# Performance work log

Measured on AMD Instinct MI355X. Metric: run time of the kernel, lower is better.

## Reference

```python
import jax, jax.numpy as jnp
import numpy as np

DIM = 1024
N_HEADS = 16
SCALE = (DIM // N_HEADS) ** (-0.5)


def setup_inputs() -> dict:
    key = jax.random.key(0)
    kq, kk, kv = jax.random.split(key, 3)
    shape = (4, 16, 2048, 64)  # [B, H, N, Dh]
    q = jax.random.normal(kq, shape, dtype=jnp.float32)
    k = jax.random.normal(kk, shape, dtype=jnp.float32)
    v = jax.random.normal(kv, shape, dtype=jnp.float32)
    return {"q": q, "k": k, "v": v}


def reference(q, k, v):
    # Faithful translation of the torch module, INCLUDING its einsum output
    # subscripts: the second einsum is 'bhnm,bhmd->bhmd' (sums over n, keeps m),
    # exactly as written in the source.
    scores = jnp.einsum('bhnd,bhmd->bhnm', q, k) * SCALE  # [B,H,N,M]
    scores = jax.nn.softmax(scores, axis=-1)
    out = jnp.einsum('bhnm,bhmd->bhmd', scores, v)  # [B,H,M,Dh]
    return out
```

## Files before the change

### kernel.cpp

```cpp
#include <hip/hip_runtime.h>
#include <cstdint>
#include <cstddef>

#define B_    4
#define H_    16
#define N_    2048
#define D_    64
#define BH_   (B_*H_)
#define SCALE 0.125f
#define QSCL  0.18033688011f

#define P_    256
#define T_    128
#define NT    (N_/T_)
#define NP    (N_/P_)
#define TILEB 16384
#define BHB   (NT*TILEB)

typedef __attribute__((ext_vector_type(8))) short bf16x8;
typedef __attribute__((ext_vector_type(4))) float f32x4;

#if __has_builtin(__builtin_amdgcn_exp2f)
#define EXP2(x) __builtin_amdgcn_exp2f(x)
#else
#define EXP2(x) exp2f(x)
#endif

__device__ __forceinline__ short f2bf(float f) {
    union { float f; unsigned u; } x; x.f = f;
    unsigned r = x.u + 0x7FFF + ((x.u >> 16) & 1);
    return (short)(r >> 16);
}

__device__ __forceinline__ size_t swz(int row, int cc) {
    return ((size_t)(row >> 7) * TILEB) + ((row & 127) << 7) + ((cc ^ (row & 7)) << 4);
}

__global__ __launch_bounds__(512)
void mha_convert(const float* __restrict__ q, const float* __restrict__ k,
                 char* __restrict__ qk)
{
    const int gid = blockIdx.x * 512 + threadIdx.x;
    const int half = BH_ * N_ * 8;
    const bool isq = gid < half;
    const float* src = isq ? q : k;
    const float scl = isq ? QSCL : 1.0f;
    char* dst = qk + (isq ? 0 : (size_t)BH_ * BHB);
    const int id = isq ? gid : gid - half;
    const int bh  = id >> 14;
    const int row = (id >> 3) & 2047;
    const int cc  = id & 7;
    const float* p = src + ((size_t)bh * N_ + row) * D_ + cc * 8;
    float4 a = *(const float4*)p;
    float4 b = *(const float4*)(p + 4);
    bf16x8 o;
    o[0] = f2bf(a.x * scl); o[1] = f2bf(a.y * scl);
    o[2] = f2bf(a.z * scl); o[3] = f2bf(a.w * scl);
    o[4] = f2bf(b.x * scl); o[5] = f2bf(b.y * scl);
    o[6] = f2bf(b.z * scl); o[7] = f2bf(b.w * scl);
    *(bf16x8*)(dst + (size_t)bh * BHB + swz(row, cc)) = o;
}

__global__ __launch_bounds__(512)
void mha_rowsum2(const char* __restrict__ qk, float* __restrict__ rinv)
{
    __shared__ __align__(16) char KT[TILEB];

    const int t = threadIdx.x, w = t >> 6, l = t & 63;
    const int wid = (blockIdx.x & 7) * 64 + (blockIdx.x >> 3);
    const int bh = wid / NP, rb = wid % NP;

    const char* Qp = qk + (size_t)bh * BHB;
    const char* Kp = qk + (size_t)BH_ * BHB + (size_t)bh * BHB;

    bf16x8 af[2][2];
    #pragma unroll
    for (int rg = 0; rg < 2; ++rg)
        #pragma unroll
        for (int kh = 0; kh < 2; ++kh) {
            int row = rb * P_ + w * 32 + rg * 16 + (l & 15);
            af[rg][kh] = *(const bf16x8*)(Qp + swz(row, kh * 4 + (l >> 4)));
        }

    float rs[2][4] = {};

    for (int ct = 0; ct < NT; ++ct) {
        __syncthreads();
        const char* src = Kp + (size_t)ct * TILEB;
        *(bf16x8*)(KT + t * 16)        = *(const bf16x8*)(src + t * 16);
        *(bf16x8*)(KT + 8192 + t * 16) = *(const bf16x8*)(src + 8192 + t * 16);
        __syncthreads();

        #pragma unroll
        for (int cj = 0; cj < 8; ++cj) {
            const int krow = cj * 16 + (l & 15);
            const int kb = (krow & 127) << 7;
            bf16x8 b0 = *(const bf16x8*)(KT + kb + (((l >> 4) ^ (krow & 7)) << 4));
            bf16x8 b1 = *(const bf16x8*)(KT + kb + (((4 + (l >> 4)) ^ (krow & 7)) << 4));
            #pragma unroll
            for (int rg = 0; rg < 2; ++rg) {
                f32x4 c = {0.f, 0.f, 0.f, 0.f};
                c = __builtin_amdgcn_mfma_f32_16x16x32_bf16(af[rg][0], b0, c, 0, 0, 0);
                c = __builtin_amdgcn_mfma_f32_16x16x32_bf16(af[rg][1], b1, c, 0, 0, 0);
                rs[rg][0] += EXP2(c[0]);
                rs[rg][1] += EXP2(c[1]);
                rs[rg][2] += EXP2(c[2]);
                rs[rg][3] += EXP2(c[3]);
            }
        }
    }

    #pragma unroll
    for (int rg = 0; rg < 2; ++rg)
        #pragma unroll
        for (int i = 0; i < 4; ++i) {
            rs[rg][i] += __shfl_xor(rs[rg][i], 1);
            rs[rg][i] += __shfl_xor(rs[rg][i], 2);
            rs[rg][i] += __shfl_xor(rs[rg][i], 4);
            rs[rg][i] += __shfl_xor(rs[rg][i], 8);
        }
    if ((l & 15) == 0) {
        #pragma unroll
        for (int rg = 0; rg < 2; ++rg) {
            const int rbase = rb * P_ + w * 32 + rg * 16 + (l >> 4) * 4;
            #pragma unroll
            for (int i = 0; i < 4; ++i)
                rinv[(size_t)bh * N_ + rbase + i] = 1.0f / rs[rg][i];
        }
    }
}

__global__ __launch_bounds__(512)
void mha_colsum2(const char* __restrict__ qk, const float* __restrict__ rinv,
                 const float* __restrict__ v, float* __restrict__ out)
{
    __shared__ __align__(16) char QT[TILEB];
    __shared__ float rv[T_];
    __shared__ float cs[P_];

    const int t = threadIdx.x, w = t >> 6, l = t & 63;
    const int wid = (blockIdx.x & 7) * 64 + (blockIdx.x >> 3);
    const int bh = wid / NP, cb = wid % NP;

    const char* Qp = qk + (size_t)bh * BHB;
    const char* Kp = qk + (size_t)BH_ * BHB + (size_t)bh * BHB;
    const float* Rg = rinv + (size_t)bh * N_;

    bf16x8 kf[2][2];
    #pragma unroll
    for (int rg = 0; rg < 2; ++rg)
        #pragma unroll
        for (int kh = 0; kh < 2; ++kh) {
            int col = cb * P_ + w * 32 + rg * 16 + (l & 15);
            kf[rg][kh] = *(const bf16x8*)(Kp + swz(col, kh * 4 + (l >> 4)));
        }

    float ca[2] = {0.f, 0.f};

    for (int rt = 0; rt < NT; ++rt) {
        __syncthreads();
        const char* src = Qp + (size_t)rt * TILEB;
        *(bf16x8*)(QT + t * 16)        = *(const bf16x8*)(src + t * 16);
        *(bf16x8*)(QT + 8192 + t * 16) = *(const bf16x8*)(src + 8192 + t * 16);
        if (t < T_) rv[t] = Rg[rt * T_ + t];
        __syncthreads();

        #pragma unroll
        for (int rj = 0; rj < 8; ++rj) {
            const int qr = rj * 16 + (l & 15);
            const int qb = (qr & 127) << 7;
            bf16x8 a0 = *(const bf16x8*)(QT + qb + (((l >> 4) ^ (qr & 7)) << 4));
            bf16x8 a1 = *(const bf16x8*)(QT + qb + (((4 + (l >> 4)) ^ (qr & 7)) << 4));
            float4 r4 = *(const float4*)&rv[rj * 16 + (l >> 4) * 4];
            #pragma unroll
            for (int rg = 0; rg < 2; ++rg) {
                f32x4 c = {0.f, 0.f, 0.f, 0.f};
                c = __builtin_amdgcn_mfma_f32_16x16x32_bf16(a0, kf[rg][0], c, 0, 0, 0);
                c = __builtin_amdgcn_mfma_f32_16x16x32_bf16(a1, kf[rg][1], c, 0, 0, 0);
                ca[rg] += EXP2(c[0]) * r4.x + EXP2(c[1]) * r4.y
                        + EXP2(c[2]) * r4.z + EXP2(c[3]) * r4.w;
            }
        }
    }

    #pragma unroll
    for (int rg = 0; rg < 2; ++rg) {
        ca[rg] += __shfl_xor(ca[rg], 16);
        ca[rg] += __shfl_xor(ca[rg], 32);
    }
    if (l < 16) { cs[w * 32 + l] = ca[0]; cs[w * 32 + 16 + l] = ca[1]; }
    __syncthreads();

    const float4* Vg = (const float4*)(v + ((size_t)bh * N_ + cb * P_) * D_);
    float4* Og = (float4*)(out + ((size_t)bh * N_ + cb * P_) * D_);
    #pragma unroll
    for (int i = 0; i < 8; ++i) {
        int id = i * 512 + t;
        float s = cs[id >> 4];
        float4 vv = Vg[id];
        float4 o; o.x = vv.x * s; o.y = vv.y * s; o.z = vv.z * s; o.w = vv.w * s;
        Og[id] = o;
    }
}

#define FTS 128
#define FNT 16

__device__ __forceinline__ bf16x8 cvt8(const float* p) {
    float4 a = *(const float4*)p;
    float4 b = *(const float4*)(p + 4);
    bf16x8 r;
    r[0] = f2bf(a.x); r[1] = f2bf(a.y); r[2] = f2bf(a.z); r[3] = f2bf(a.w);
    r[4] = f2bf(b.x); r[5] = f2bf(b.y); r[6] = f2bf(b.z); r[7] = f2bf(b.w);
    return r;
}
__device__ __forceinline__ void fstage(char* lds, const float* src, int t) {
    #pragma unroll
    for (int i = 0; i < 2; ++i) {
        int ch = i * 512 + t, r = ch >> 3, cc = ch & 7;
        bf16x8 v = cvt8(src + (size_t)r * D_ + cc * 8);
        *(bf16x8*)(lds + r * 128 + ((cc ^ (r & 7)) << 4)) = v;
    }
}
__device__ __forceinline__ bf16x8 fread(const char* lds, int row, int cc) {
    return *(const bf16x8*)(lds + row * 128 + ((cc ^ (row & 7)) << 4));
}

__global__ __launch_bounds__(512)
void mha_rowsum_fb(const float* __restrict__ q, const float* __restrict__ k,
                   float* __restrict__ rinv)
{
    __shared__ __align__(16) char KT[FTS * 128];
    const int t = threadIdx.x, w = t >> 6, l = t & 63;
    const int bh = blockIdx.x / FNT, rb = blockIdx.x % FNT;
    const float* Qg = q + (size_t)bh * N_ * D_;
    const float* Kg = k + (size_t)bh * N_ * D_;
    const int qrow = rb * FTS + w * 16 + (l & 15);
    bf16x8 af[2];
    #pragma unroll
    for (int kh = 0; kh < 2; ++kh)
        af[kh] = cvt8(Qg + (size_t)qrow * D_ + kh * 32 + (l >> 4) * 8);
    float rs[4] = {0.f, 0.f, 0.f, 0.f};
    for (int ct = 0; ct < FNT; ++ct) {
        __syncthreads();
        fstage(KT, Kg + (size_t)ct * FTS * D_, t);
        __syncthreads();
        #pragma unroll
        for (int cj = 0; cj < 8; ++cj) {
            const int krow = cj * 16 + (l & 15);
            f32x4 c = {0.f, 0.f, 0.f, 0.f};
            #pragma unroll
            for (int kh = 0; kh < 2; ++kh)
                c = __builtin_amdgcn_mfma_f32_16x16x32_bf16(af[kh], fread(KT, krow, kh * 4 + (l >> 4)), c, 0, 0, 0);
            rs[0] += __expf(c[0] * SCALE); rs[1] += __expf(c[1] * SCALE);
            rs[2] += __expf(c[2] * SCALE); rs[3] += __expf(c[3] * SCALE);
        }
    }
    #pragma unroll
    for (int i = 0; i < 4; ++i) {
        rs[i] += __shfl_xor(rs[i], 1); rs[i] += __shfl_xor(rs[i], 2);
        rs[i] += __shfl_xor(rs[i], 4); rs[i] += __shfl_xor(rs[i], 8);
    }
    if ((l & 15) == 0) {
        const int rbase = rb * FTS + w * 16 + (l >> 4) * 4;
        #pragma unroll
        for (int i = 0; i < 4; ++i)
            rinv[(size_t)bh * N_ + rbase + i] = 1.0f / rs[i];
    }
}

__global__ __launch_bounds__(512)
void mha_colsum_fb(const float* __restrict__ q, const float* __restrict__ k,
                   const float* __restrict__ v, const float* __restrict__ rinv,
                   float* __restrict__ out)
{
    __shared__ __align__(16) char QT[FTS * 128];
    __shared__ float rv[FTS];
    __shared__ float cs[FTS];
    const int t = threadIdx.x, w = t >> 6, l = t & 63;
    const int bh = blockIdx.x / FNT, cb = blockIdx.x % FNT;
    const float* Qg = q + (size_t)bh * N_ * D_;
    const float* Kg = k + (size_t)bh * N_ * D_;
    const float* Rg = rinv + (size_t)bh * N_;
    const int kcol = cb * FTS + w * 16 + (l & 15);
    bf16x8 kf[2];
    #pragma unroll
    for (int kh = 0; kh < 2; ++kh)
        kf[kh] = cvt8(Kg + (size_t)kcol * D_ + kh * 32 + (l >> 4) * 8);
    float ca = 0.f;
    for (int rt = 0; rt < FNT; ++rt) {
        __syncthreads();
        fstage(QT, Qg + (size_t)rt * FTS * D_, t);
        if (t < FTS) rv[t] = Rg[rt * FTS + t];
        __syncthreads();
        #pragma unroll
        for (int rj = 0; rj < 8; ++rj) {
            const int qr = rj * 16 + (l & 15);
            f32x4 c = {0.f, 0.f, 0.f, 0.f};
            #pragma unroll
            for (int kh = 0; kh < 2; ++kh)
                c = __builtin_amdgcn_mfma_f32_16x16x32_bf16(fread(QT, qr, kh * 4 + (l >> 4)), kf[kh], c, 0, 0, 0);
            float4 r4 = *(const float4*)&rv[rj * 16 + (l >> 4) * 4];
            ca += __expf(c[0] * SCALE) * r4.x + __expf(c[1] * SCALE) * r4.y
                + __expf(c[2] * SCALE) * r4.z + __expf(c[3] * SCALE) * r4.w;
        }
    }
    ca += __shfl_xor(ca, 16); ca += __shfl_xor(ca, 32);
    if (l < 16) cs[w * 16 + l] = ca;
    __syncthreads();
    const float4* Vg = (const float4*)(v + (size_t)bh * N_ * D_ + (size_t)cb * FTS * D_);
    float4* Og = (float4*)(out + (size_t)bh * N_ * D_ + (size_t)cb * FTS * D_);
    #pragma unroll
    for (int i = 0; i < 4; ++i) {
        int id = i * 512 + t;
        float s = cs[id >> 4];
        float4 vv = Vg[id];
        float4 o; o.x = vv.x * s; o.y = vv.y * s; o.z = vv.z * s; o.w = vv.w * s;
        Og[id] = o;
    }
}

extern "C" void kernel_launch(void* const* d_in, const int* in_sizes, int n_in,
                              void* d_out, int out_size, void* d_ws, size_t ws_size,
                              hipStream_t stream)
{
    const float* q = (const float*)d_in[0];
    const float* k = (const float*)d_in[1];
    const float* v = (const float*)d_in[2];
    float* out = (float*)d_out;

    const size_t qkBytes = (size_t)2 * BH_ * BHB;
    const size_t need = qkBytes + (size_t)BH_ * N_ * 4;

    if (ws_size >= need) {
        char* qk = (char*)d_ws;
        float* rinv = (float*)(qk + qkBytes);
        mha_convert<<<dim3(2 * BH_ * N_ * 8 / 512), dim3(512), 0, stream>>>(q, k, qk);
        mha_rowsum2<<<dim3(BH_ * NP), dim3(512), 0, stream>>>(qk, rinv);
        mha_colsum2<<<dim3(BH_ * NP), dim3(512), 0, stream>>>(qk, rinv, v, out);
    } else {
        float* rinv = (float*)d_ws;
        mha_rowsum_fb<<<dim3(BH_ * FNT), dim3(512), 0, stream>>>(q, k, rinv);
        mha_colsum_fb<<<dim3(BH_ * FNT), dim3(512), 0, stream>>>(q, k, v, rinv, out);
    }
}
```

Measured before the change: 108.4 us.

## Double-buffer K/Q tiles via direct global-to-LDS loads and halve rows per block

```diff
diff --git a/kernel.cpp b/kernel.cpp
--- a/kernel.cpp
+++ b/kernel.cpp
@@ -10,10 +10,10 @@
 #define SCALE 0.125f
 #define QSCL  0.18033688011f
 
-#define P_    256
-#define T_    128
-#define NT    (N_/T_)
-#define NP    (N_/P_)
+#define P2    128
+#define T2    128
+#define NT    (N_/T2)
+#define NP2   (N_/P2)
 #define TILEB 16384
 #define BHB   (NT*TILEB)
 
@@ -34,6 +34,12 @@
 
 __device__ __forceinline__ size_t swz(int row, int cc) {
     return ((size_t)(row >> 7) * TILEB) + ((row & 127) << 7) + ((cc ^ (row & 7)) << 4);
+}
+
+__device__ __forceinline__ void gload_lds16(const char* g, char* l) {
+    __builtin_amdgcn_global_load_lds(
+        (const __attribute__((address_space(1))) void*)g,
+        (__attribute__((address_space(3))) void*)l, 16, 0, 0);
 }
 
 __global__ __launch_bounds__(512)
@@ -62,139 +68,137 @@
 }
 
 __global__ __launch_bounds__(512)
-void mha_rowsum2(const char* __restrict__ qk, float* __restrict__ rinv)
-{
-    __shared__ __align__(16) char KT[TILEB];
+void mha_rowsum3(const char* __restrict__ qk, float* __restrict__ rinv)
+{
+    __shared__ __align__(16) char KT[2][TILEB];
 
     const int t = threadIdx.x, w = t >> 6, l = t & 63;
-    const int wid = (blockIdx.x & 7) * 64 + (blockIdx.x >> 3);
-    const int bh = wid / NP, rb = wid % NP;
+    const int wid = (blockIdx.x & 7) * 128 + (blockIdx.x >> 3);
+    const int bh = wid >> 4, rb = wid & 15;
 
     const char* Qp = qk + (size_t)bh * BHB;
     const char* Kp = qk + (size_t)BH_ * BHB + (size_t)bh * BHB;
 
-    bf16x8 af[2][2];
-    #pragma unroll
-    for (int rg = 0; rg < 2; ++rg)
-        #pragma unroll
-        for (int kh = 0; kh < 2; ++kh) {
-            int row = rb * P_ + w * 32 + rg * 16 + (l & 15);
-            af[rg][kh] = *(const bf16x8*)(Qp + swz(row, kh * 4 + (l >> 4)));
-        }
-
-    float rs[2][4] = {};
-
-    for (int ct = 0; ct < NT; ++ct) {
-        __syncthreads();
-        const char* src = Kp + (size_t)ct * TILEB;
-        *(bf16x8*)(KT + t * 16)        = *(const bf16x8*)(src + t * 16);
-        *(bf16x8*)(KT + 8192 + t * 16) = *(const bf16x8*)(src + 8192 + t * 16);
-        __syncthreads();
-
+    bf16x8 af[2];
+    #pragma unroll
+    for (int kh = 0; kh < 2; ++kh)
+        af[kh] = *(const bf16x8*)(Qp + swz(rb * P2 + w * 16 + (l & 15), kh * 4 + (l >> 4)));
+
+    float rs[4] = {0.f, 0.f, 0.f, 0.f};
+
+    auto compute = [&](const char* kt) {
         #pragma unroll
         for (int cj = 0; cj < 8; ++cj) {
             const int krow = cj * 16 + (l & 15);
             const int kb = (krow & 127) << 7;
-            bf16x8 b0 = *(const bf16x8*)(KT + kb + (((l >> 4) ^ (krow & 7)) << 4));
-            bf16x8 b1 = *(const bf16x8*)(KT + kb + (((4 + (l >> 4)) ^ (krow & 7)) << 4));
-            #pragma unroll
-            for (int rg = 0; rg < 2; ++rg) {
-                f32x4 c = {0.f, 0.f, 0.f, 0.f};
-                c = __builtin_amdgcn_mfma_f32_16x16x32_bf16(af[rg][0], b0, c, 0, 0, 0);
-                c = __builtin_amdgcn_mfma_f32_16x16x32_bf16(af[rg][1], b1, c, 0, 0, 0);
-                rs[rg][0] += EXP2(c[0]);
-                rs[rg][1] += EXP2(c[1]);
-                rs[rg][2] += EXP2(c[2]);
-                rs[rg][3] += EXP2(c[3]);
-            }
+            bf16x8 b0 = *(const bf16x8*)(kt + kb + (((l >> 4) ^ (krow & 7)) << 4));
+            bf16x8 b1 = *(const bf16x8*)(kt + kb + (((4 + (l >> 4)) ^ (krow & 7)) << 4));
+            f32x4 c = {0.f, 0.f, 0.f, 0.f};
+            c = __builtin_amdgcn_mfma_f32_16x16x32_bf16(af[0], b0, c, 0, 0, 0);
+            c = __builtin_amdgcn_mfma_f32_16x16x32_bf16(af[1], b1, c, 0, 0, 0);
+            rs[0] += EXP2(c[0]);
+            rs[1] += EXP2(c[1]);
+            rs[2] += EXP2(c[2]);
+            rs[3] += EXP2(c[3]);
         }
-    }
-
-    #pragma unroll
-    for (int rg = 0; rg < 2; ++rg)
-        #pragma unroll
-        for (int i = 0; i < 4; ++i) {
-            rs[rg][i] += __shfl_xor(rs[rg][i], 1);
-            rs[rg][i] += __shfl_xor(rs[rg][i], 2);
-            rs[rg][i] += __shfl_xor(rs[rg][i], 4);
-            rs[rg][i] += __shfl_xor(rs[rg][i], 8);
-        }
+    };
+
+    gload_lds16(Kp + t * 16,        KT[0] + t * 16);
+    gload_lds16(Kp + 8192 + t * 16, KT[0] + 8192 + t * 16);
+    __syncthreads();
+
+    #pragma unroll 1
+    for (int ct = 0; ct < NT - 1; ++ct) {
+        const char* src = Kp + (size_t)(ct + 1) * TILEB;
+        char* dst = KT[(ct + 1) & 1];
+        gload_lds16(src + t * 16,        dst + t * 16);
+        gload_lds16(src + 8192 + t * 16, dst + 8192 + t * 16);
+        compute(KT[ct & 1]);
+        __syncthreads();
+    }
+    compute(KT[(NT - 1) & 1]);
+
+    #pragma unroll
+    for (int i = 0; i < 4; ++i) {
+        rs[i] += __shfl_xor(rs[i], 1);
+        rs[i] += __shfl_xor(rs[i], 2);
+        rs[i] += __shfl_xor(rs[i], 4);
+        rs[i] += __shfl_xor(rs[i], 8);
+    }
     if ((l & 15) == 0) {
-        #pragma unroll
-        for (int rg = 0; rg < 2; ++rg) {
-            const int rbase = rb * P_ + w * 32 + rg * 16 + (l >> 4) * 4;
-            #pragma unroll
-            for (int i = 0; i < 4; ++i)
-                rinv[(size_t)bh * N_ + rbase + i] = 1.0f / rs[rg][i];
-        }
-    }
-}
-
-__global__ __launch_bounds__(512)
-void mha_colsum2(const char* __restrict__ qk, const float* __restrict__ rinv,
+        const int rbase = rb * P2 + w * 16 + (l >> 4) * 4;
+        #pragma unroll
+        for (int i = 0; i < 4; ++i)
+            rinv[(size_t)bh * N_ + rbase + i] = 1.0f / rs[i];
+    }
+}
+
+__global__ __launch_bounds__(512)
+void mha_colsum3(const char* __restrict__ qk, const float* __restrict__ rinv,
                  const float* __restrict__ v, float* __restrict__ out)
 {
-    __shared__ __align__(16) char QT[TILEB];
-    __shared__ float rv[T_];
-    __shared__ float cs[P_];
+    __shared__ __align__(16) char QT[2][TILEB];
+    __shared__ float rv[2][T2];
+    __shared__ float cs[P2];
 
     const int t = threadIdx.x, w = t >> 6, l = t & 63;
-    const int wid = (blockIdx.x & 7) * 64 + (blockIdx.x >> 3);
-    const int bh = wid / NP, cb = wid % NP;
+    const int wid = (blockIdx.x & 7) * 128 + (blockIdx.x >> 3);
+    const int bh = wid >> 4, cb = wid & 15;
 
     const char* Qp = qk + (size_t)bh * BHB;
     const char* Kp = qk + (size_t)BH_ * BHB + (size_t)bh * BHB;
     const float* Rg = rinv + (size_t)bh * N_;
 
-    bf16x8 kf[2][2];
-    #pragma unroll
-    for (int rg = 0; rg < 2; ++rg)
-        #pragma unroll
-        for (int kh = 0; kh < 2; ++kh) {
-            int col = cb * P_ + w * 32 + rg * 16 + (l & 15);
-            kf[rg][kh] = *(const bf16x8*)(Kp + swz(col, kh * 4 + (l >> 4)));
-        }
-
-    float ca[2] = {0.f, 0.f};
-
-    for (int rt = 0; rt < NT; ++rt) {
-        __syncthreads();
-        const char* src = Qp + (size_t)rt * TILEB;
-        *(bf16x8*)(QT + t * 16)        = *(const bf16x8*)(src + t * 16);
-        *(bf16x8*)(QT + 8192 + t * 16) = *(const bf16x8*)(src + 8192 + t * 16);
-        if (t < T_) rv[t] = Rg[rt * T_ + t];
-        __syncthreads();
-
+    bf16x8 kf[2];
+    #pragma unroll
+    for (int kh = 0; kh < 2; ++kh)
+        kf[kh] = *(const bf16x8*)(Kp + swz(cb * P2 + w * 16 + (l & 15), kh * 4 + (l >> 4)));
+
+    float ca = 0.f;
+
+    auto compute = [&](const char* qt, const float* rvb) {
         #pragma unroll
         for (int rj = 0; rj < 8; ++rj) {
             const int qr = rj * 16 + (l & 15);
             const int qb = (qr & 127) << 7;
-            bf16x8 a0 = *(const bf16x8*)(QT + qb + (((l >> 4) ^ (qr & 7)) << 4));
-            bf16x8 a1 = *(const bf16x8*)(QT + qb + (((4 + (l >> 4)) ^ (qr & 7)) << 4));
-            float4 r4 = *(const float4*)&rv[rj * 16 + (l >> 4) * 4];
-            #pragma unroll
-            for (int rg = 0; rg < 2; ++rg) {
-                f32x4 c = {0.f, 0.f, 0.f, 0.f};
-                c = __builtin_amdgcn_mfma_f32_16x16x32_bf16(a0, kf[rg][0], c, 0, 0, 0);
-                c = __builtin_amdgcn_mfma_f32_16x16x32_bf16(a1, kf[rg][1], c, 0, 0, 0);
-                ca[rg] += EXP2(c[0]) * r4.x + EXP2(c[1]) * r4.y
-                        + EXP2(c[2]) * r4.z + EXP2(c[3]) * r4.w;
-            }
+            bf16x8 a0 = *(const bf16x8*)(qt + qb + (((l >> 4) ^ (qr & 7)) << 4));
+            bf16x8 a1 = *(const bf16x8*)(qt + qb + (((4 + (l >> 4)) ^ (qr & 7)) << 4));
+            float4 r4 = *(const float4*)&rvb[rj * 16 + (l >> 4) * 4];
+            f32x4 c = {0.f, 0.f, 0.f, 0.f};
+            c = __builtin_amdgcn_mfma_f32_16x16x32_bf16(a0, kf[0], c, 0, 0, 0);
+            c = __builtin_amdgcn_mfma_f32_16x16x32_bf16(a1, kf[1], c, 0, 0, 0);
+            ca += EXP2(c[0]) * r4.x + EXP2(c[1]) * r4.y
+                + EXP2(c[2]) * r4.z + EXP2(c[3]) * r4.w;
         }
-    }
-
-    #pragma unroll
-    for (int rg = 0; rg < 2; ++rg) {
-        ca[rg] += __shfl_xor(ca[rg], 16);
-        ca[rg] += __shfl_xor(ca[rg], 32);
-    }
-    if (l < 16) { cs[w * 32 + l] = ca[0]; cs[w * 32 + 16 + l] = ca[1]; }
+    };
+
+    gload_lds16(Qp + t * 16,        QT[0] + t * 16);
+    gload_lds16(Qp + 8192 + t * 16, QT[0] + 8192 + t * 16);
+    if (t < T2) rv[0][t] = Rg[t];
     __syncthreads();
 
-    const float4* Vg = (const float4*)(v + ((size_t)bh * N_ + cb * P_) * D_);
-    float4* Og = (float4*)(out + ((size_t)bh * N_ + cb * P_) * D_);
-    #pragma unroll
-    for (int i = 0; i < 8; ++i) {
+    #pragma unroll 1
+    for (int rt = 0; rt < NT - 1; ++rt) {
+        const int nxt = (rt + 1) & 1;
+        const char* src = Qp + (size_t)(rt + 1) * TILEB;
+        char* dst = QT[nxt];
+        gload_lds16(src + t * 16,        dst + t * 16);
+        gload_lds16(src + 8192 + t * 16, dst + 8192 + t * 16);
+        if (t < T2) rv[nxt][t] = Rg[(rt + 1) * T2 + t];
+        compute(QT[rt & 1], rv[rt & 1]);
+        __syncthreads();
+    }
+    compute(QT[(NT - 1) & 1], rv[(NT - 1) & 1]);
+
+    ca += __shfl_xor(ca, 16);
+    ca += __shfl_xor(ca, 32);
+    if (l < 16) cs[w * 16 + l] = ca;
+    __syncthreads();
+
+    const float4* Vg = (const float4*)(v + ((size_t)bh * N_ + cb * P2) * D_);
+    float4* Og = (float4*)(out + ((size_t)bh * N_ + cb * P2) * D_);
+    #pragma unroll
+    for (int i = 0; i < 4; ++i) {
         int id = i * 512 + t;
         float s = cs[id >> 4];
         float4 vv = Vg[id];
@@ -336,8 +340,8 @@
         char* qk = (char*)d_ws;
         float* rinv = (float*)(qk + qkBytes);
         mha_convert<<<dim3(2 * BH_ * N_ * 8 / 512), dim3(512), 0, stream>>>(q, k, qk);
-        mha_rowsum2<<<dim3(BH_ * NP), dim3(512), 0, stream>>>(qk, rinv);
-        mha_colsum2<<<dim3(BH_ * NP), dim3(512), 0, stream>>>(qk, rinv, v, out);
+        mha_rowsum3<<<dim3(BH_ * NP2), dim3(512), 0, stream>>>(qk, rinv);
+        mha_colsum3<<<dim3(BH_ * NP2), dim3(512), 0, stream>>>(qk, rinv, v, out);
     } else {
         float* rinv = (float*)d_ws;
         mha_rowsum_fb<<<dim3(BH_ * FNT), dim3(512), 0, stream>>>(q, k, rinv);
```

Result: slower. 115.8 us (+6.8%).

## Double-buffer LDS tiles with direct global-to-LDS loads and smaller blocks

Applied to the files above, without the earlier changes.

```diff
diff --git a/kernel.cpp b/kernel.cpp
--- a/kernel.cpp
+++ b/kernel.cpp
@@ -10,10 +10,10 @@
 #define SCALE 0.125f
 #define QSCL  0.18033688011f
 
-#define P_    256
-#define T_    128
-#define NT    (N_/T_)
-#define NP    (N_/P_)
+#define P3    128
+#define T3    128
+#define NT    (N_/T3)
+#define NP3   (N_/P3)
 #define TILEB 16384
 #define BHB   (NT*TILEB)
 
@@ -34,6 +34,12 @@
 
 __device__ __forceinline__ size_t swz(int row, int cc) {
     return ((size_t)(row >> 7) * TILEB) + ((row & 127) << 7) + ((cc ^ (row & 7)) << 4);
+}
+
+__device__ __forceinline__ void gload_lds16(const char* g, char* l) {
+    __builtin_amdgcn_global_load_lds(
+        (const __attribute__((address_space(1))) void*)g,
+        (__attribute__((address_space(3))) void*)l, 16, 0, 0);
 }
 
 __global__ __launch_bounds__(512)
@@ -61,14 +67,14 @@
     *(bf16x8*)(dst + (size_t)bh * BHB + swz(row, cc)) = o;
 }
 
-__global__ __launch_bounds__(512)
-void mha_rowsum2(const char* __restrict__ qk, float* __restrict__ rinv)
-{
-    __shared__ __align__(16) char KT[TILEB];
+__global__ __launch_bounds__(256)
+void mha_rowsum4(const char* __restrict__ qk, float* __restrict__ rinv)
+{
+    __shared__ __align__(16) char KT[2][TILEB];
 
     const int t = threadIdx.x, w = t >> 6, l = t & 63;
-    const int wid = (blockIdx.x & 7) * 64 + (blockIdx.x >> 3);
-    const int bh = wid / NP, rb = wid % NP;
+    const int wid = (blockIdx.x & 7) * 128 + (blockIdx.x >> 3);
+    const int bh = wid >> 4, rb = wid & 15;
 
     const char* Qp = qk + (size_t)bh * BHB;
     const char* Kp = qk + (size_t)BH_ * BHB + (size_t)bh * BHB;
@@ -77,26 +83,28 @@
     #pragma unroll
     for (int rg = 0; rg < 2; ++rg)
         #pragma unroll
-        for (int kh = 0; kh < 2; ++kh) {
-            int row = rb * P_ + w * 32 + rg * 16 + (l & 15);
-            af[rg][kh] = *(const bf16x8*)(Qp + swz(row, kh * 4 + (l >> 4)));
-        }
+        for (int kh = 0; kh < 2; ++kh)
+            af[rg][kh] = *(const bf16x8*)(Qp + swz(rb * P3 + w * 32 + rg * 16 + (l & 15),
+                                                   kh * 4 + (l >> 4)));
+
+    const int lb0 = (l & 15) * 128 + (((l >> 4) ^ (l & 7)) << 4);
+    const int lb1 = (l & 15) * 128 + (((4 + (l >> 4)) ^ (l & 7)) << 4);
 
     float rs[2][4] = {};
 
-    for (int ct = 0; ct < NT; ++ct) {
-        __syncthreads();
+    auto stage = [&](int ct, int buf) {
         const char* src = Kp + (size_t)ct * TILEB;
-        *(bf16x8*)(KT + t * 16)        = *(const bf16x8*)(src + t * 16);
-        *(bf16x8*)(KT + 8192 + t * 16) = *(const bf16x8*)(src + 8192 + t * 16);
-        __syncthreads();
-
+        char* dst = KT[buf];
+        #pragma unroll
+        for (int i = 0; i < 4; ++i)
+            gload_lds16(src + i * 4096 + t * 16, dst + i * 4096 + t * 16);
+    };
+
+    auto compute = [&](const char* kt) {
         #pragma unroll
         for (int cj = 0; cj < 8; ++cj) {
-            const int krow = cj * 16 + (l & 15);
-            const int kb = (krow & 127) << 7;
-            bf16x8 b0 = *(const bf16x8*)(KT + kb + (((l >> 4) ^ (krow & 7)) << 4));
-            bf16x8 b1 = *(const bf16x8*)(KT + kb + (((4 + (l >> 4)) ^ (krow & 7)) << 4));
+            bf16x8 b0 = *(const bf16x8*)(kt + lb0 + cj * 2048);
+            bf16x8 b1 = *(const bf16x8*)(kt + lb1 + cj * 2048);
             #pragma unroll
             for (int rg = 0; rg < 2; ++rg) {
                 f32x4 c = {0.f, 0.f, 0.f, 0.f};
@@ -108,7 +116,18 @@
                 rs[rg][3] += EXP2(c[3]);
             }
         }
-    }
+    };
+
+    stage(0, 0);
+    __syncthreads();
+
+    #pragma unroll 1
+    for (int ct = 0; ct < NT - 1; ++ct) {
+        stage(ct + 1, (ct + 1) & 1);
+        compute(KT[ct & 1]);
+        __syncthreads();
+    }
+    compute(KT[(NT - 1) & 1]);
 
     #pragma unroll
     for (int rg = 0; rg < 2; ++rg)
@@ -122,7 +141,7 @@
     if ((l & 15) == 0) {
         #pragma unroll
         for (int rg = 0; rg < 2; ++rg) {
-            const int rbase = rb * P_ + w * 32 + rg * 16 + (l >> 4) * 4;
+            const int rbase = rb * P3 + w * 32 + rg * 16 + (l >> 4) * 4;
             #pragma unroll
             for (int i = 0; i < 4; ++i)
                 rinv[(size_t)bh * N_ + rbase + i] = 1.0f / rs[rg][i];
@@ -130,17 +149,17 @@
     }
 }
 
-__global__ __launch_bounds__(512)
-void mha_colsum2(const char* __restrict__ qk, const float* __restrict__ rinv,
+__global__ __launch_bounds__(256)
+void mha_colsum4(const char* __restrict__ qk, const float* __restrict__ rinv,
                  const float* __restrict__ v, float* __restrict__ out)
 {
-    __shared__ __align__(16) char QT[TILEB];
-    __shared__ float rv[T_];
-    __shared__ float cs[P_];
+    __shared__ __align__(16) char QT[2][TILEB];
+    __shared__ float rv[2][T3];
+    __shared__ float cs[P3];
 
     const int t = threadIdx.x, w = t >> 6, l = t & 63;
-    const int wid = (blockIdx.x & 7) * 64 + (blockIdx.x >> 3);
-    const int bh = wid / NP, cb = wid % NP;
+    const int wid = (blockIdx.x & 7) * 128 + (blockIdx.x >> 3);
+    const int bh = wid >> 4, cb = wid & 15;
 
     const char* Qp = qk + (size_t)bh * BHB;
     const char* Kp = qk + (size_t)BH_ * BHB + (size_t)bh * BHB;
@@ -150,28 +169,30 @@
     #pragma unroll
     for (int rg = 0; rg < 2; ++rg)
         #pragma unroll
-        for (int kh = 0; kh < 2; ++kh) {
-            int col = cb * P_ + w * 32 + rg * 16 + (l & 15);
-            kf[rg][kh] = *(const bf16x8*)(Kp + swz(col, kh * 4 + (l >> 4)));
-        }
+        for (int kh = 0; kh < 2; ++kh)
+            kf[rg][kh] = *(const bf16x8*)(Kp + swz(cb * P3 + w * 32 + rg * 16 + (l & 15),
+                                                    kh * 4 + (l >> 4)));
+
+    const int lb0 = (l & 15) * 128 + (((l >> 4) ^ (l & 7)) << 4);
+    const int lb1 = (l & 15) * 128 + (((4 + (l >> 4)) ^ (l & 7)) << 4);
 
     float ca[2] = {0.f, 0.f};
 
-    for (int rt = 0; rt < NT; ++rt) {
-        __syncthreads();
+    auto stage = [&](int rt, int buf) {
         const char* src = Qp + (size_t)rt * TILEB;
-        *(bf16x8*)(QT + t * 16)        = *(const bf16x8*)(src + t * 16);
-        *(bf16x8*)(QT + 8192 + t * 16) = *(const bf16x8*)(src + 8192 + t * 16);
-        if (t < T_) rv[t] = Rg[rt * T_ + t];
-        __syncthreads();
-
+        char* dst = QT[buf];
+        #pragma unroll
+        for (int i = 0; i < 4; ++i)
+            gload_lds16(src + i * 4096 + t * 16, dst + i * 4096 + t * 16);
+        if (t < T3) rv[buf][t] = Rg[rt * T3 + t];
+    };
+
+    auto compute = [&](const char* qt, const float* rvb) {
         #pragma unroll
         for (int rj = 0; rj < 8; ++rj) {
-            const int qr = rj * 16 + (l & 15);
-            const int qb = (qr & 127) << 7;
-            bf16x8 a0 = *(const bf16x8*)(QT + qb + (((l >> 4) ^ (qr & 7)) << 4));
-            bf16x8 a1 = *(const bf16x8*)(QT + qb + (((4 + (l >> 4)) ^ (qr & 7)) << 4));
-            float4 r4 = *(const float4*)&rv[rj * 16 + (l >> 4) * 4];
+            bf16x8 a0 = *(const bf16x8*)(qt + lb0 + rj * 2048);
+            bf16x8 a1 = *(const bf16x8*)(qt + lb1 + rj * 2048);
+            float4 r4 = *(const float4*)&rvb[rj * 16 + (l >> 4) * 4];
             #pragma unroll
             for (int rg = 0; rg < 2; ++rg) {
                 f32x4 c = {0.f, 0.f, 0.f, 0.f};
@@ -181,7 +202,18 @@
                         + EXP2(c[2]) * r4.z + EXP2(c[3]) * r4.w;
             }
         }
-    }
+    };
+
+    stage(0, 0);
+    __syncthreads();
+
+    #pragma unroll 1
+    for (int rt = 0; rt < NT - 1; ++rt) {
+        stage(rt + 1, (rt + 1) & 1);
+        compute(QT[rt & 1], rv[rt & 1]);
+        __syncthreads();
+    }
+    compute(QT[(NT - 1) & 1], rv[(NT - 1) & 1]);
 
     #pragma unroll
     for (int rg = 0; rg < 2; ++rg) {
@@ -191,11 +223,11 @@
     if (l < 16) { cs[w * 32 + l] = ca[0]; cs[w * 32 + 16 + l] = ca[1]; }
     __syncthreads();
 
-    const float4* Vg = (const float4*)(v + ((size_t)bh * N_ + cb * P_) * D_);
-    float4* Og = (float4*)(out + ((size_t)bh * N_ + cb * P_) * D_);
+    const float4* Vg = (const float4*)(v + ((size_t)bh * N_ + cb * P3) * D_);
+    float4* Og = (float4*)(out + ((size_t)bh * N_ + cb * P3) * D_);
     #pragma unroll
     for (int i = 0; i < 8; ++i) {
-        int id = i * 512 + t;
+        int id = i * 256 + t;
         float s = cs[id >> 4];
         float4 vv = Vg[id];
         float4 o; o.x = vv.x * s; o.y = vv.y * s; o.z = vv.z * s; o.w = vv.w * s;
@@ -336,8 +368,8 @@
         char* qk = (char*)d_ws;
         float* rinv = (float*)(qk + qkBytes);
         mha_convert<<<dim3(2 * BH_ * N_ * 8 / 512), dim3(512), 0, stream>>>(q, k, qk);
-        mha_rowsum2<<<dim3(BH_ * NP), dim3(512), 0, stream>>>(qk, rinv);
-        mha_colsum2<<<dim3(BH_ * NP), dim3(512), 0, stream>>>(qk, rinv, v, out);
+        mha_rowsum4<<<dim3(BH_ * NP3), dim3(256), 0, stream>>>(qk, rinv);
+        mha_colsum4<<<dim3(BH_ * NP3), dim3(256), 0, stream>>>(qk, rinv, v, out);
     } else {
         float* rinv = (float*)d_ws;
         mha_rowsum_fb<<<dim3(BH_ * FNT), dim3(512), 0, stream>>>(q, k, rinv);
```

After: 121.8 us. 1.12x slower.

## Store Q/K in MFMA fragment-major layout and read tiles directly from global

Applied to the files above, without the earlier changes.

```diff
diff --git a/kernel.cpp b/kernel.cpp
--- a/kernel.cpp
+++ b/kernel.cpp
@@ -10,10 +10,7 @@
 #define SCALE 0.125f
 #define QSCL  0.18033688011f
 
-#define P_    256
-#define T_    128
-#define NT    (N_/T_)
-#define NP    (N_/P_)
+#define NT    16
 #define TILEB 16384
 #define BHB   (NT*TILEB)
 
@@ -32,8 +29,9 @@
     return (short)(r >> 16);
 }
 
-__device__ __forceinline__ size_t swz(int row, int cc) {
-    return ((size_t)(row >> 7) * TILEB) + ((row & 127) << 7) + ((cc ^ (row & 7)) << 4);
+__device__ __forceinline__ size_t fmaj(int row, int cc) {
+    return ((size_t)(row >> 7) * TILEB) + (((row >> 4) & 7) << 11)
+         + ((cc >> 2) << 10) + ((cc & 3) << 8) + ((row & 15) << 4);
 }
 
 __global__ __launch_bounds__(512)
@@ -58,47 +56,40 @@
     o[2] = f2bf(a.z * scl); o[3] = f2bf(a.w * scl);
     o[4] = f2bf(b.x * scl); o[5] = f2bf(b.y * scl);
     o[6] = f2bf(b.z * scl); o[7] = f2bf(b.w * scl);
-    *(bf16x8*)(dst + (size_t)bh * BHB + swz(row, cc)) = o;
-}
-
-__global__ __launch_bounds__(512)
-void mha_rowsum2(const char* __restrict__ qk, float* __restrict__ rinv)
-{
-    __shared__ __align__(16) char KT[TILEB];
-
+    *(bf16x8*)(dst + (size_t)bh * BHB + fmaj(row, cc)) = o;
+}
+
+__global__ __launch_bounds__(256)
+void mha_rowsum5(const char* __restrict__ qk, float* __restrict__ rinv)
+{
     const int t = threadIdx.x, w = t >> 6, l = t & 63;
     const int wid = (blockIdx.x & 7) * 64 + (blockIdx.x >> 3);
-    const int bh = wid / NP, rb = wid % NP;
+    const int bh = wid >> 3, rb = wid & 7;
 
     const char* Qp = qk + (size_t)bh * BHB;
     const char* Kp = qk + (size_t)BH_ * BHB + (size_t)bh * BHB;
-
-    bf16x8 af[2][2];
-    #pragma unroll
-    for (int rg = 0; rg < 2; ++rg)
-        #pragma unroll
-        for (int kh = 0; kh < 2; ++kh) {
-            int row = rb * P_ + w * 32 + rg * 16 + (l & 15);
-            af[rg][kh] = *(const bf16x8*)(Qp + swz(row, kh * 4 + (l >> 4)));
-        }
-
-    float rs[2][4] = {};
-
+    const int rbase = rb * 256 + w * 64;
+
+    bf16x8 af[4][2];
+    #pragma unroll
+    for (int rg = 0; rg < 4; ++rg) {
+        const int row0 = rbase + rg * 16;
+        const char* gb = Qp + (row0 >> 7) * TILEB + (((row0 >> 4) & 7) << 11);
+        af[rg][0] = *(const bf16x8*)(gb + l * 16);
+        af[rg][1] = *(const bf16x8*)(gb + 1024 + l * 16);
+    }
+
+    float rs[4][4] = {};
+
+    #pragma unroll 1
     for (int ct = 0; ct < NT; ++ct) {
-        __syncthreads();
-        const char* src = Kp + (size_t)ct * TILEB;
-        *(bf16x8*)(KT + t * 16)        = *(const bf16x8*)(src + t * 16);
-        *(bf16x8*)(KT + 8192 + t * 16) = *(const bf16x8*)(src + 8192 + t * 16);
-        __syncthreads();
-
-        #pragma unroll
-        for (int cj = 0; cj < 8; ++cj) {
-            const int krow = cj * 16 + (l & 15);
-            const int kb = (krow & 127) << 7;
-            bf16x8 b0 = *(const bf16x8*)(KT + kb + (((l >> 4) ^ (krow & 7)) << 4));
-            bf16x8 b1 = *(const bf16x8*)(KT + kb + (((4 + (l >> 4)) ^ (krow & 7)) << 4));
-            #pragma unroll
-            for (int rg = 0; rg < 2; ++rg) {
+        const char* tb = Kp + (size_t)ct * TILEB;
+        #pragma unroll
+        for (int g = 0; g < 8; ++g) {
+            bf16x8 b0 = *(const bf16x8*)(tb + g * 2048 + l * 16);
+            bf16x8 b1 = *(const bf16x8*)(tb + g * 2048 + 1024 + l * 16);
+            #pragma unroll
+            for (int rg = 0; rg < 4; ++rg) {
                 f32x4 c = {0.f, 0.f, 0.f, 0.f};
                 c = __builtin_amdgcn_mfma_f32_16x16x32_bf16(af[rg][0], b0, c, 0, 0, 0);
                 c = __builtin_amdgcn_mfma_f32_16x16x32_bf16(af[rg][1], b1, c, 0, 0, 0);
@@ -111,7 +102,7 @@
     }
 
     #pragma unroll
-    for (int rg = 0; rg < 2; ++rg)
+    for (int rg = 0; rg < 4; ++rg)
         #pragma unroll
         for (int i = 0; i < 4; ++i) {
             rs[rg][i] += __shfl_xor(rs[rg][i], 1);
@@ -121,59 +112,51 @@
         }
     if ((l & 15) == 0) {
         #pragma unroll
-        for (int rg = 0; rg < 2; ++rg) {
-            const int rbase = rb * P_ + w * 32 + rg * 16 + (l >> 4) * 4;
+        for (int rg = 0; rg < 4; ++rg) {
+            const int rr = rbase + rg * 16 + (l >> 4) * 4;
             #pragma unroll
             for (int i = 0; i < 4; ++i)
-                rinv[(size_t)bh * N_ + rbase + i] = 1.0f / rs[rg][i];
-        }
-    }
-}
-
-__global__ __launch_bounds__(512)
-void mha_colsum2(const char* __restrict__ qk, const float* __restrict__ rinv,
+                rinv[(size_t)bh * N_ + rr + i] = 1.0f / rs[rg][i];
+        }
+    }
+}
+
+__global__ __launch_bounds__(256)
+void mha_colsum5(const char* __restrict__ qk, const float* __restrict__ rinv,
                  const float* __restrict__ v, float* __restrict__ out)
 {
-    __shared__ __align__(16) char QT[TILEB];
-    __shared__ float rv[T_];
-    __shared__ float cs[P_];
+    __shared__ float cs[256];
 
     const int t = threadIdx.x, w = t >> 6, l = t & 63;
     const int wid = (blockIdx.x & 7) * 64 + (blockIdx.x >> 3);
-    const int bh = wid / NP, cb = wid % NP;
+    const int bh = wid >> 3, cb = wid & 7;
 
     const char* Qp = qk + (size_t)bh * BHB;
     const char* Kp = qk + (size_t)BH_ * BHB + (size_t)bh * BHB;
     const float* Rg = rinv + (size_t)bh * N_;
-
-    bf16x8 kf[2][2];
-    #pragma unroll
-    for (int rg = 0; rg < 2; ++rg)
-        #pragma unroll
-        for (int kh = 0; kh < 2; ++kh) {
-            int col = cb * P_ + w * 32 + rg * 16 + (l & 15);
-            kf[rg][kh] = *(const bf16x8*)(Kp + swz(col, kh * 4 + (l >> 4)));
-        }
-
-    float ca[2] = {0.f, 0.f};
-
+    const int cbase = cb * 256 + w * 64;
+
+    bf16x8 kf[4][2];
+    #pragma unroll
+    for (int rg = 0; rg < 4; ++rg) {
+        const int col0 = cbase + rg * 16;
+        const char* gb = Kp + (col0 >> 7) * TILEB + (((col0 >> 4) & 7) << 11);
+        kf[rg][0] = *(const bf16x8*)(gb + l * 16);
+        kf[rg][1] = *(const bf16x8*)(gb + 1024 + l * 16);
+    }
+
+    float ca[4] = {0.f, 0.f, 0.f, 0.f};
+
+    #pragma unroll 1
     for (int rt = 0; rt < NT; ++rt) {
-        __syncthreads();
-        const char* src = Qp + (size_t)rt * TILEB;
-        *(bf16x8*)(QT + t * 16)        = *(const bf16x8*)(src + t * 16);
-        *(bf16x8*)(QT + 8192 + t * 16) = *(const bf16x8*)(src + 8192 + t * 16);
-        if (t < T_) rv[t] = Rg[rt * T_ + t];
-        __syncthreads();
-
-        #pragma unroll
-        for (int rj = 0; rj < 8; ++rj) {
-            const int qr = rj * 16 + (l & 15);
-            const int qb = (qr & 127) << 7;
-            bf16x8 a0 = *(const bf16x8*)(QT + qb + (((l >> 4) ^ (qr & 7)) << 4));
-            bf16x8 a1 = *(const bf16x8*)(QT + qb + (((4 + (l >> 4)) ^ (qr & 7)) << 4));
-            float4 r4 = *(const float4*)&rv[rj * 16 + (l >> 4) * 4];
-            #pragma unroll
-            for (int rg = 0; rg < 2; ++rg) {
+        const char* tb = Qp + (size_t)rt * TILEB;
+        #pragma unroll
+        for (int g = 0; g < 8; ++g) {
+            bf16x8 a0 = *(const bf16x8*)(tb + g * 2048 + l * 16);
+            bf16x8 a1 = *(const bf16x8*)(tb + g * 2048 + 1024 + l * 16);
+            float4 r4 = *(const float4*)(Rg + rt * 128 + g * 16 + (l >> 4) * 4);
+            #pragma unroll
+            for (int rg = 0; rg < 4; ++rg) {
                 f32x4 c = {0.f, 0.f, 0.f, 0.f};
                 c = __builtin_amdgcn_mfma_f32_16x16x32_bf16(a0, kf[rg][0], c, 0, 0, 0);
                 c = __builtin_amdgcn_mfma_f32_16x16x32_bf16(a1, kf[rg][1], c, 0, 0, 0);
@@ -184,18 +167,18 @@
     }
 
     #pragma unroll
-    for (int rg = 0; rg < 2; ++rg) {
+    for (int rg = 0; rg < 4; ++rg) {
         ca[rg] += __shfl_xor(ca[rg], 16);
         ca[rg] += __shfl_xor(ca[rg], 32);
-    }
-    if (l < 16) { cs[w * 32 + l] = ca[0]; cs[w * 32 + 16 + l] = ca[1]; }
+        if (l < 16) cs[w * 64 + rg * 16 + l] = ca[rg];
+    }
     __syncthreads();
 
-    const float4* Vg = (const float4*)(v + ((size_t)bh * N_ + cb * P_) * D_);
-    float4* Og = (float4*)(out + ((size_t)bh * N_ + cb * P_) * D_);
-    #pragma unroll
-    for (int i = 0; i < 8; ++i) {
-        int id = i * 512 + t;
+    const float4* Vg = (const float4*)(v + ((size_t)bh * N_ + cb * 256) * D_);
+    float4* Og = (float4*)(out + ((size_t)bh * N_ + cb * 256) * D_);
+    #pragma unroll
+    for (int i = 0; i < 16; ++i) {
+        int id = i * 256 + t;
         float s = cs[id >> 4];
         float4 vv = Vg[id];
         float4 o; o.x = vv.x * s; o.y = vv.y * s; o.z = vv.z * s; o.w = vv.w * s;
@@ -336,8 +319,8 @@
         char* qk = (char*)d_ws;
         float* rinv = (float*)(qk + qkBytes);
         mha_convert<<<dim3(2 * BH_ * N_ * 8 / 512), dim3(512), 0, stream>>>(q, k, qk);
-        mha_rowsum2<<<dim3(BH_ * NP), dim3(512), 0, stream>>>(qk, rinv);
-        mha_colsum2<<<dim3(BH_ * NP), dim3(512), 0, stream>>>(qk, rinv, v, out);
+        mha_rowsum5<<<dim3(BH_ * 8), dim3(256), 0, stream>>>(qk, rinv);
+        mha_colsum5<<<dim3(BH_ * 8), dim3(256), 0, stream>>>(qk, rinv, v, out);
     } else {
         float* rinv = (float*)d_ws;
         mha_rowsum_fb<<<dim3(BH_ * FNT), dim3(512), 0, stream>>>(q, k, rinv);
```

Result: slower. 210.3 us (+94.0%).
